# Performance work log

Hardware: AMD Instinct MI355X
Metric: run time of the kernel (lower is better)

The kernel has to match this reference:

```python
import jax, jax.numpy as jnp
import numpy as np

NUM_CODES = 512
DIM = 64
B, M = 32, 64


def setup_inputs() -> dict:
    key = jax.random.key(0)
    k1, k2 = jax.random.split(key)
    inputs = jax.random.normal(k1, (B, M, M, DIM), dtype=jnp.float32)
    # keras 'uniform' initializer is U(-0.05, 0.05)
    embeddings = jax.random.uniform(k2, (NUM_CODES, DIM), dtype=jnp.float32,
                                    minval=-0.05, maxval=0.05)
    return {"inputs": inputs, "embeddings": embeddings}


def reference(inputs, embeddings):
    l2_inputs = jnp.sum(inputs * inputs, axis=-1, keepdims=True)      # [B,M,M,1]
    l2_embeddings = jnp.sum(embeddings * embeddings, axis=-1)          # [K]
    dot = jnp.einsum('bhwd,kd->bhwk', inputs, embeddings)              # [B,M,M,K]
    distance = l2_inputs + l2_embeddings - 2.0 * dot                   # [B,M,M,K]
    codes = jnp.argmin(distance, axis=-1).astype(jnp.int32)            # [B,M,M]
    code_vecs = embeddings[codes]                                      # [B,M,M,D]
    return codes, code_vecs
```

## Files before the change

kernel.cpp:

```cpp
#include <hip/hip_runtime.h>

#define NUM_CODES 512
#define DIM 64
#define NPIX (32 * 64 * 64)
#define CT (NUM_CODES / 16)
#define BLK 256
#define NGRP 2
#define PPB 128

typedef __attribute__((ext_vector_type(8))) short bf16x8;
typedef __attribute__((ext_vector_type(4))) float f32x4;

__device__ __forceinline__ unsigned short f2bf(float f) {
    unsigned u = __float_as_uint(f);
    return (unsigned short)((u + 0x7fffu + ((u >> 16) & 1u)) >> 16);
}
__device__ __forceinline__ float bf2f(unsigned short h) {
    return __uint_as_float(((unsigned)h) << 16);
}

__global__ __launch_bounds__(256) void prep_kernel(
    const float* __restrict__ emb, unsigned short* __restrict__ AH,
    unsigned short* __restrict__ ALO, float* __restrict__ l2e,
    float* __restrict__ l2eh) {
    const int t = blockIdx.x * 256 + threadIdx.x;
    const int e0 = t * 4;
    const int c = e0 >> 6, d0 = e0 & 63;
    const float4 v = *(const float4*)(emb + c * DIM + d0);
    float f[4] = {-v.x, -v.y, -v.z, -v.w};
    unsigned short h[4], l[4];
#pragma unroll
    for (int i = 0; i < 4; ++i) {
        h[i] = f2bf(f[i]);
        l[i] = f2bf(f[i] - bf2f(h[i]));
    }
    const int ct = c >> 4, mr = c & 15, s = d0 >> 5, q = (d0 & 31) >> 3,
              j0 = d0 & 7;
    const int base = ((ct * 2 + s) * 64 + (q * 16 + mr)) * 8 + j0;
    *(ushort4*)(AH + base) = make_ushort4(h[0], h[1], h[2], h[3]);
    *(ushort4*)(ALO + base) = make_ushort4(l[0], l[1], l[2], l[3]);

    if (t < NUM_CODES) {
        const float* e = emb + t * DIM;
        float r[8];
#pragma unroll
        for (int j = 0; j < 8; ++j) {
            float w = e[j];
            r[j] = w * w;
        }
#pragma unroll
        for (int i = 8; i < DIM; i += 8)
#pragma unroll
            for (int j = 0; j < 8; ++j) {
                float w = e[i + j];
                r[j] += w * w;
            }
        float sv =
            ((r[0] + r[1]) + (r[2] + r[3])) + ((r[4] + r[5]) + (r[6] + r[7]));
        l2e[t] = sv;
        l2eh[t] = 0.5f * sv;
    }
}

__global__ __launch_bounds__(BLK, 4) void vq_main(
    const float* __restrict__ x_in, const unsigned short* __restrict__ AH,
    const unsigned short* __restrict__ ALO, const float* __restrict__ l2e,
    const float* __restrict__ l2eh, const float* __restrict__ emb,
    float* __restrict__ codes_out, float* __restrict__ vecs_out) {
    __shared__ float s_l2eh[NUM_CODES];
    __shared__ float s_l2ex[NUM_CODES];
    __shared__ int s_top[PPB][2];
    __shared__ int s_code[PPB];

    const int tid = threadIdx.x, lane = tid & 63, wave = tid >> 6;
    s_l2eh[tid] = l2eh[tid];
    s_l2eh[tid + 256] = l2eh[tid + 256];
    s_l2ex[tid] = l2e[tid];
    s_l2ex[tid + 256] = l2e[tid + 256];
    __syncthreads();

    const int p = lane & 15, q = lane >> 4;
    const int pw = blockIdx.x * PPB + wave * (16 * NGRP);

    bf16x8 bh0[NGRP], bl0[NGRP], bh1[NGRP], bl1[NGRP];
#pragma unroll
    for (int g = 0; g < NGRP; ++g) {
        const float* xb = x_in + (size_t)(pw + g * 16 + p) * DIM + q * 8;
        float4 u0 = *(const float4*)(xb);
        float4 u1 = *(const float4*)(xb + 4);
        float4 u2 = *(const float4*)(xb + 32);
        float4 u3 = *(const float4*)(xb + 36);
        float f0[8] = {u0.x, u0.y, u0.z, u0.w, u1.x, u1.y, u1.z, u1.w};
        float f1[8] = {u2.x, u2.y, u2.z, u2.w, u3.x, u3.y, u3.z, u3.w};
#pragma unroll
        for (int j = 0; j < 8; ++j) {
            unsigned short hh = f2bf(f0[j]);
            bh0[g][j] = (short)hh;
            bl0[g][j] = (short)f2bf(f0[j] - bf2f(hh));
            unsigned short h2 = f2bf(f1[j]);
            bh1[g][j] = (short)h2;
            bl1[g][j] = (short)f2bf(f1[j] - bf2f(h2));
        }
    }

    const int rowbase = q * 4;
    float d1[NGRP], d2[NGRP];
    int k1[NGRP], k2[NGRP];
#pragma unroll
    for (int g = 0; g < NGRP; ++g) {
        d1[g] = 3.4e38f;
        d2[g] = 3.4e38f;
        k1[g] = 0;
        k2[g] = 0;
    }

    const unsigned short* pAH = AH + lane * 8;
    const unsigned short* pAL = ALO + lane * 8;

    bf16x8 c0h = *(const bf16x8*)(pAH);
    bf16x8 c0l = *(const bf16x8*)(pAL);
    bf16x8 c1h = *(const bf16x8*)(pAH + 512);
    bf16x8 c1l = *(const bf16x8*)(pAL + 512);
    bf16x8 p0h = *(const bf16x8*)(pAH + 1024);
    bf16x8 p0l = *(const bf16x8*)(pAL + 1024);
    bf16x8 p1h = *(const bf16x8*)(pAH + 1024 + 512);
    bf16x8 p1l = *(const bf16x8*)(pAL + 1024 + 512);

#pragma unroll 4
    for (int ct = 0; ct < CT; ++ct) {
        const int nt = (ct + 2) & (CT - 1);
        const bf16x8 q0h = *(const bf16x8*)(pAH + nt * 1024);
        const bf16x8 q0l = *(const bf16x8*)(pAL + nt * 1024);
        const bf16x8 q1h = *(const bf16x8*)(pAH + nt * 1024 + 512);
        const bf16x8 q1l = *(const bf16x8*)(pAL + nt * 1024 + 512);

        const int kb = ct * 16 + rowbase;
        const f32x4 acc_init = *(const f32x4*)&s_l2eh[kb];

        f32x4 accA[NGRP], accB[NGRP];
        __builtin_amdgcn_s_setprio(1);
#pragma unroll
        for (int g = 0; g < NGRP; ++g) {
            f32x4 a = acc_init;
            a = __builtin_amdgcn_mfma_f32_16x16x32_bf16(c0h, bh0[g], a, 0, 0, 0);
            a = __builtin_amdgcn_mfma_f32_16x16x32_bf16(c0l, bh0[g], a, 0, 0, 0);
            a = __builtin_amdgcn_mfma_f32_16x16x32_bf16(c0h, bl0[g], a, 0, 0, 0);
            f32x4 b = {0.f, 0.f, 0.f, 0.f};
            b = __builtin_amdgcn_mfma_f32_16x16x32_bf16(c1h, bh1[g], b, 0, 0, 0);
            b = __builtin_amdgcn_mfma_f32_16x16x32_bf16(c1l, bh1[g], b, 0, 0, 0);
            b = __builtin_amdgcn_mfma_f32_16x16x32_bf16(c1h, bl1[g], b, 0, 0, 0);
            accA[g] = a;
            accB[g] = b;
        }
        __builtin_amdgcn_s_setprio(0);

#pragma unroll
        for (int g = 0; g < NGRP; ++g) {
#pragma unroll
            for (int r = 0; r < 4; ++r) {
                const float d = accA[g][r] + accB[g][r];
                const int kk = kb + r;
                const bool c = d < d1[g], c2 = d < d2[g];
                const float nd2 = __builtin_amdgcn_fmed3f(d1[g], d2[g], d);
                const int nk2 = c2 ? kk : k2[g];
                k2[g] = c ? k1[g] : nk2;
                k1[g] = c ? kk : k1[g];
                d2[g] = nd2;
                d1[g] = fminf(d1[g], d);
            }
        }

        c0h = p0h; c0l = p0l; c1h = p1h; c1l = p1l;
        p0h = q0h; p0l = q0l; p1h = q1h; p1l = q1l;
    }

#pragma unroll
    for (int g = 0; g < NGRP; ++g) {
        float a1 = d1[g], a2 = d2[g];
        int b1 = k1[g], b2 = k2[g];
#pragma unroll
        for (int off = 16; off <= 32; off <<= 1) {
            const float od1 = __shfl_xor(a1, off);
            const int ok1 = __shfl_xor(b1, off);
            const float od2 = __shfl_xor(a2, off);
            const int ok2 = __shfl_xor(b2, off);
            const bool c = od1 < a1;
            const float w1 = c ? od1 : a1;
            const int wk1 = c ? ok1 : b1;
            const float l1 = c ? a1 : od1;
            const int lk1 = c ? b1 : ok1;
            const bool cm = od2 < a2;
            const float m2 = cm ? od2 : a2;
            const int mk2 = cm ? ok2 : b2;
            const bool c3 = m2 < l1;
            a2 = c3 ? m2 : l1;
            b2 = c3 ? mk2 : lk1;
            a1 = w1;
            b1 = wk1;
        }
        if (lane < 16) {
            const int pb = wave * (16 * NGRP) + g * 16 + lane;
            s_top[pb][0] = b1;
            s_top[pb][1] = b2;
        }
    }
    __syncthreads();

    {
        const int pixloc = tid >> 1, which = tid & 1;
        const int pix = blockIdx.x * PPB + pixloc;
        const int k_me = s_top[pixloc][which];
        const float* xr = x_in + (size_t)pix * DIM;
        float x[DIM];
#pragma unroll
        for (int jj = 0; jj < 16; ++jj) {
            const float4 v = *(const float4*)(xr + jj * 4);
            x[4 * jj + 0] = v.x;
            x[4 * jj + 1] = v.y;
            x[4 * jj + 2] = v.z;
            x[4 * jj + 3] = v.w;
        }
        float r[8];
#pragma unroll
        for (int j = 0; j < 8; ++j) r[j] = x[j] * x[j];
#pragma unroll
        for (int i = 8; i < DIM; i += 8)
#pragma unroll
            for (int j = 0; j < 8; ++j) r[j] += x[i + j] * x[i + j];
        const float l2x =
            ((r[0] + r[1]) + (r[2] + r[3])) + ((r[4] + r[5]) + (r[6] + r[7]));

        const float* em = emb + (size_t)k_me * DIM;
        float acc = 0.f;
#pragma unroll
        for (int d = 0; d < DIM; ++d) acc = __builtin_fmaf(x[d], em[d], acc);
        const float d_me = (l2x + s_l2ex[k_me]) - 2.0f * acc;

        const float d_o = __shfl_xor(d_me, 1);
        const int k_o = __shfl_xor(k_me, 1);
        const int sel =
            (d_me < d_o || (d_me == d_o && k_me < k_o)) ? k_me : k_o;
        if (which == 0) {
            s_code[pixloc] = sel;
            codes_out[pix] = (float)sel;
        }
    }
    __syncthreads();

    const float4* emb4 = (const float4*)emb;
    float4* vout4 = (float4*)(vecs_out + (size_t)blockIdx.x * PPB * DIM);
#pragma unroll
    for (int it = 0; it < (PPB * DIM / 4) / BLK; ++it) {
        const int fidx = tid + it * BLK;
        const int pp = fidx >> 4, dd = fidx & 15;
        vout4[fidx] = emb4[(size_t)s_code[pp] * (DIM / 4) + dd];
    }
}

extern "C" void kernel_launch(void* const* d_in, const int* in_sizes, int n_in,
                              void* d_out, int out_size, void* d_ws,
                              size_t ws_size, hipStream_t stream) {
    const float* x_in = (const float*)d_in[0];
    const float* emb = (const float*)d_in[1];

    unsigned short* AH = (unsigned short*)d_ws;
    unsigned short* ALO = AH + NUM_CODES * DIM;
    float* l2e = (float*)(ALO + NUM_CODES * DIM);
    float* l2eh = l2e + NUM_CODES;

    float* codes_out = (float*)d_out;
    float* vecs_out = (float*)d_out + NPIX;

    hipLaunchKernelGGL(prep_kernel, dim3(32), dim3(256), 0, stream, emb, AH,
                       ALO, l2e, l2eh);
    hipLaunchKernelGGL(vq_main, dim3(NPIX / PPB), dim3(BLK), 0, stream, x_in,
                       AH, ALO, l2e, l2eh, emb, codes_out, vecs_out);
}
```

Measured before the change: 120.1 us.

## Switch to single-wave blocks with shuffle-based exchange, removing LDS and barriers

Each block becomes one 64-lane wave processing 16 pixels instead of four waves with two pixel groups each. Shared-memory staging of norms, top-2 candidates and codes is replaced by direct global loads of the code norms and cross-lane shuffles, which removes all block-level barriers. The intent is to cut synchronisation and LDS overhead and raise occupancy. In exchange, each codebook fragment loaded is reused across half as many pixels, so codebook reads double and each wave has less independent MFMA work to hide latency.

```diff
diff --git a/kernel.cpp b/kernel.cpp
--- a/kernel.cpp
+++ b/kernel.cpp
@@ -4,9 +4,8 @@
 #define DIM 64
 #define NPIX (32 * 64 * 64)
 #define CT (NUM_CODES / 16)
-#define BLK 256
-#define NGRP 2
-#define PPB 128
+#define BLK 64
+#define PPB 16
 
 typedef __attribute__((ext_vector_type(8))) short bf16x8;
 typedef __attribute__((ext_vector_type(4))) float f32x4;
@@ -62,30 +61,18 @@
     }
 }
 
-__global__ __launch_bounds__(BLK, 4) void vq_main(
+__global__ __launch_bounds__(BLK, 8) void vq_main(
     const float* __restrict__ x_in, const unsigned short* __restrict__ AH,
     const unsigned short* __restrict__ ALO, const float* __restrict__ l2e,
     const float* __restrict__ l2eh, const float* __restrict__ emb,
     float* __restrict__ codes_out, float* __restrict__ vecs_out) {
-    __shared__ float s_l2eh[NUM_CODES];
-    __shared__ float s_l2ex[NUM_CODES];
-    __shared__ int s_top[PPB][2];
-    __shared__ int s_code[PPB];
-
-    const int tid = threadIdx.x, lane = tid & 63, wave = tid >> 6;
-    s_l2eh[tid] = l2eh[tid];
-    s_l2eh[tid + 256] = l2eh[tid + 256];
-    s_l2ex[tid] = l2e[tid];
-    s_l2ex[tid + 256] = l2e[tid + 256];
-    __syncthreads();
-
+    const int lane = threadIdx.x;
     const int p = lane & 15, q = lane >> 4;
-    const int pw = blockIdx.x * PPB + wave * (16 * NGRP);
-
-    bf16x8 bh0[NGRP], bl0[NGRP], bh1[NGRP], bl1[NGRP];
-#pragma unroll
-    for (int g = 0; g < NGRP; ++g) {
-        const float* xb = x_in + (size_t)(pw + g * 16 + p) * DIM + q * 8;
+    const int pw = blockIdx.x * PPB;
+
+    bf16x8 bh0, bl0, bh1, bl1;
+    {
+        const float* xb = x_in + (size_t)(pw + p) * DIM + q * 8;
         float4 u0 = *(const float4*)(xb);
         float4 u1 = *(const float4*)(xb + 4);
         float4 u2 = *(const float4*)(xb + 32);
@@ -95,36 +82,32 @@
 #pragma unroll
         for (int j = 0; j < 8; ++j) {
             unsigned short hh = f2bf(f0[j]);
-            bh0[g][j] = (short)hh;
-            bl0[g][j] = (short)f2bf(f0[j] - bf2f(hh));
+            bh0[j] = (short)hh;
+            bl0[j] = (short)f2bf(f0[j] - bf2f(hh));
             unsigned short h2 = f2bf(f1[j]);
-            bh1[g][j] = (short)h2;
-            bl1[g][j] = (short)f2bf(f1[j] - bf2f(h2));
+            bh1[j] = (short)h2;
+            bl1[j] = (short)f2bf(f1[j] - bf2f(h2));
         }
     }
 
     const int rowbase = q * 4;
-    float d1[NGRP], d2[NGRP];
-    int k1[NGRP], k2[NGRP];
-#pragma unroll
-    for (int g = 0; g < NGRP; ++g) {
-        d1[g] = 3.4e38f;
-        d2[g] = 3.4e38f;
-        k1[g] = 0;
-        k2[g] = 0;
-    }
+    float d1 = 3.4e38f, d2 = 3.4e38f;
+    int k1 = 0, k2 = 0;
 
     const unsigned short* pAH = AH + lane * 8;
     const unsigned short* pAL = ALO + lane * 8;
+    const float* pL = l2eh + rowbase;
 
     bf16x8 c0h = *(const bf16x8*)(pAH);
     bf16x8 c0l = *(const bf16x8*)(pAL);
     bf16x8 c1h = *(const bf16x8*)(pAH + 512);
     bf16x8 c1l = *(const bf16x8*)(pAL + 512);
+    f32x4 ci = *(const f32x4*)(pL);
     bf16x8 p0h = *(const bf16x8*)(pAH + 1024);
     bf16x8 p0l = *(const bf16x8*)(pAL + 1024);
     bf16x8 p1h = *(const bf16x8*)(pAH + 1024 + 512);
     bf16x8 p1l = *(const bf16x8*)(pAL + 1024 + 512);
+    f32x4 pi = *(const f32x4*)(pL + 16);
 
 #pragma unroll 4
     for (int ct = 0; ct < CT; ++ct) {
@@ -133,51 +116,40 @@
         const bf16x8 q0l = *(const bf16x8*)(pAL + nt * 1024);
         const bf16x8 q1h = *(const bf16x8*)(pAH + nt * 1024 + 512);
         const bf16x8 q1l = *(const bf16x8*)(pAL + nt * 1024 + 512);
+        const f32x4 qi = *(const f32x4*)(pL + nt * 16);
+
+        __builtin_amdgcn_s_setprio(1);
+        f32x4 a = ci;
+        a = __builtin_amdgcn_mfma_f32_16x16x32_bf16(c0h, bh0, a, 0, 0, 0);
+        a = __builtin_amdgcn_mfma_f32_16x16x32_bf16(c0l, bh0, a, 0, 0, 0);
+        a = __builtin_amdgcn_mfma_f32_16x16x32_bf16(c0h, bl0, a, 0, 0, 0);
+        f32x4 b = {0.f, 0.f, 0.f, 0.f};
+        b = __builtin_amdgcn_mfma_f32_16x16x32_bf16(c1h, bh1, b, 0, 0, 0);
+        b = __builtin_amdgcn_mfma_f32_16x16x32_bf16(c1l, bh1, b, 0, 0, 0);
+        b = __builtin_amdgcn_mfma_f32_16x16x32_bf16(c1h, bl1, b, 0, 0, 0);
+        __builtin_amdgcn_s_setprio(0);
 
         const int kb = ct * 16 + rowbase;
-        const f32x4 acc_init = *(const f32x4*)&s_l2eh[kb];
-
-        f32x4 accA[NGRP], accB[NGRP];
-        __builtin_amdgcn_s_setprio(1);
-#pragma unroll
-        for (int g = 0; g < NGRP; ++g) {
-            f32x4 a = acc_init;
-            a = __builtin_amdgcn_mfma_f32_16x16x32_bf16(c0h, bh0[g], a, 0, 0, 0);
-            a = __builtin_amdgcn_mfma_f32_16x16x32_bf16(c0l, bh0[g], a, 0, 0, 0);
-            a = __builtin_amdgcn_mfma_f32_16x16x32_bf16(c0h, bl0[g], a, 0, 0, 0);
-            f32x4 b = {0.f, 0.f, 0.f, 0.f};
-            b = __builtin_amdgcn_mfma_f32_16x16x32_bf16(c1h, bh1[g], b, 0, 0, 0);
-            b = __builtin_amdgcn_mfma_f32_16x16x32_bf16(c1l, bh1[g], b, 0, 0, 0);
-            b = __builtin_amdgcn_mfma_f32_16x16x32_bf16(c1h, bl1[g], b, 0, 0, 0);
-            accA[g] = a;
-            accB[g] = b;
-        }
-        __builtin_amdgcn_s_setprio(0);
-
-#pragma unroll
-        for (int g = 0; g < NGRP; ++g) {
-#pragma unroll
-            for (int r = 0; r < 4; ++r) {
-                const float d = accA[g][r] + accB[g][r];
-                const int kk = kb + r;
-                const bool c = d < d1[g], c2 = d < d2[g];
-                const float nd2 = __builtin_amdgcn_fmed3f(d1[g], d2[g], d);
-                const int nk2 = c2 ? kk : k2[g];
-                k2[g] = c ? k1[g] : nk2;
-                k1[g] = c ? kk : k1[g];
-                d2[g] = nd2;
-                d1[g] = fminf(d1[g], d);
-            }
-        }
-
-        c0h = p0h; c0l = p0l; c1h = p1h; c1l = p1l;
-        p0h = q0h; p0l = q0l; p1h = q1h; p1l = q1l;
-    }
-
-#pragma unroll
-    for (int g = 0; g < NGRP; ++g) {
-        float a1 = d1[g], a2 = d2[g];
-        int b1 = k1[g], b2 = k2[g];
+#pragma unroll
+        for (int r = 0; r < 4; ++r) {
+            const float d = a[r] + b[r];
+            const int kk = kb + r;
+            const bool c = d < d1, c2 = d < d2;
+            const float nd2 = __builtin_amdgcn_fmed3f(d1, d2, d);
+            const int nk2 = c2 ? kk : k2;
+            k2 = c ? k1 : nk2;
+            k1 = c ? kk : k1;
+            d2 = nd2;
+            d1 = fminf(d1, d);
+        }
+
+        c0h = p0h; c0l = p0l; c1h = p1h; c1l = p1l; ci = pi;
+        p0h = q0h; p0l = q0l; p1h = q1h; p1l = q1l; pi = qi;
+    }
+
+    {
+        float a1 = d1, a2 = d2;
+        int b1 = k1, b2 = k2;
 #pragma unroll
         for (int off = 16; off <= 32; off <<= 1) {
             const float od1 = __shfl_xor(a1, off);
@@ -198,62 +170,69 @@
             a1 = w1;
             b1 = wk1;
         }
-        if (lane < 16) {
-            const int pb = wave * (16 * NGRP) + g * 16 + lane;
-            s_top[pb][0] = b1;
-            s_top[pb][1] = b2;
-        }
-    }
-    __syncthreads();
-
+        d1 = a1; k1 = b1;
+        d2 = a2; k2 = b2;
+    }
+
+    int sel;
     {
-        const int pixloc = tid >> 1, which = tid & 1;
-        const int pix = blockIdx.x * PPB + pixloc;
-        const int k_me = s_top[pixloc][which];
-        const float* xr = x_in + (size_t)pix * DIM;
-        float x[DIM];
-#pragma unroll
-        for (int jj = 0; jj < 16; ++jj) {
-            const float4 v = *(const float4*)(xr + jj * 4);
-            x[4 * jj + 0] = v.x;
-            x[4 * jj + 1] = v.y;
-            x[4 * jj + 2] = v.z;
-            x[4 * jj + 3] = v.w;
-        }
-        float r[8];
-#pragma unroll
-        for (int j = 0; j < 8; ++j) r[j] = x[j] * x[j];
-#pragma unroll
-        for (int i = 8; i < DIM; i += 8)
-#pragma unroll
-            for (int j = 0; j < 8; ++j) r[j] += x[i + j] * x[i + j];
-        const float l2x =
-            ((r[0] + r[1]) + (r[2] + r[3])) + ((r[4] + r[5]) + (r[6] + r[7]));
-
-        const float* em = emb + (size_t)k_me * DIM;
-        float acc = 0.f;
-#pragma unroll
-        for (int d = 0; d < DIM; ++d) acc = __builtin_fmaf(x[d], em[d], acc);
-        const float d_me = (l2x + s_l2ex[k_me]) - 2.0f * acc;
-
+        const int pixloc = (lane >> 1) & 15, which = lane & 1;
+        const int ka = __shfl(k1, pixloc);
+        const int kb2 = __shfl(k2, pixloc);
+        const int k_me = which ? kb2 : ka;
+        float d_me = 3.4e38f;
+        if (lane < 32) {
+            const int pix = pw + pixloc;
+            const float* xr = x_in + (size_t)pix * DIM;
+            const float* er = emb + (size_t)k_me * DIM;
+            float r[8];
+            float acc = 0.f;
+#pragma unroll
+            for (int i = 0; i < DIM; i += 8) {
+                const float4 xa = *(const float4*)(xr + i);
+                const float4 xb2 = *(const float4*)(xr + i + 4);
+                const float4 ea = *(const float4*)(er + i);
+                const float4 eb = *(const float4*)(er + i + 4);
+                if (i == 0) {
+                    r[0] = xa.x * xa.x; r[1] = xa.y * xa.y;
+                    r[2] = xa.z * xa.z; r[3] = xa.w * xa.w;
+                    r[4] = xb2.x * xb2.x; r[5] = xb2.y * xb2.y;
+                    r[6] = xb2.z * xb2.z; r[7] = xb2.w * xb2.w;
+                } else {
+                    r[0] += xa.x * xa.x; r[1] += xa.y * xa.y;
+                    r[2] += xa.z * xa.z; r[3] += xa.w * xa.w;
+                    r[4] += xb2.x * xb2.x; r[5] += xb2.y * xb2.y;
+                    r[6] += xb2.z * xb2.z; r[7] += xb2.w * xb2.w;
+                }
+                acc = __builtin_fmaf(xa.x, ea.x, acc);
+                acc = __builtin_fmaf(xa.y, ea.y, acc);
+                acc = __builtin_fmaf(xa.z, ea.z, acc);
+                acc = __builtin_fmaf(xa.w, ea.w, acc);
+                acc = __builtin_fmaf(xb2.x, eb.x, acc);
+                acc = __builtin_fmaf(xb2.y, eb.y, acc);
+                acc = __builtin_fmaf(xb2.z, eb.z, acc);
+                acc = __builtin_fmaf(xb2.w, eb.w, acc);
+            }
+            const float l2x = ((r[0] + r[1]) + (r[2] + r[3])) +
+                              ((r[4] + r[5]) + (r[6] + r[7]));
+            d_me = (l2x + l2e[k_me]) - 2.0f * acc;
+        }
         const float d_o = __shfl_xor(d_me, 1);
         const int k_o = __shfl_xor(k_me, 1);
-        const int sel =
-            (d_me < d_o || (d_me == d_o && k_me < k_o)) ? k_me : k_o;
-        if (which == 0) {
-            s_code[pixloc] = sel;
-            codes_out[pix] = (float)sel;
-        }
-    }
-    __syncthreads();
+        sel = (d_me < d_o || (d_me == d_o && k_me < k_o)) ? k_me : k_o;
+        if (lane < 32 && which == 0) {
+            codes_out[pw + pixloc] = (float)sel;
+        }
+    }
 
     const float4* emb4 = (const float4*)emb;
     float4* vout4 = (float4*)(vecs_out + (size_t)blockIdx.x * PPB * DIM);
 #pragma unroll
     for (int it = 0; it < (PPB * DIM / 4) / BLK; ++it) {
-        const int fidx = tid + it * BLK;
+        const int fidx = lane + it * BLK;
         const int pp = fidx >> 4, dd = fidx & 15;
-        vout4[fidx] = emb4[(size_t)s_code[pp] * (DIM / 4) + dd];
+        const int cpp = __shfl(sel, pp * 2);
+        vout4[fidx] = emb4[(size_t)cpp * (DIM / 4) + dd];
     }
 }
 
```

New measurement: 380.5 us. 3.17x slower.

## Stage codebook tiles through LDS with double-buffered global_load_lds

Applied to the files above, without the earlier changes.

Replaces per-wave register prefetching of codebook hi/lo bf16 fragments from global memory with a block-cooperative double-buffered LDS staging scheme using global_load_lds. Each wave loads one quarter of the next tile directly into shared memory, then all waves read fragments from LDS. The aim is to cut redundant global/L2 traffic, since every wave previously fetched the full codebook, and to free VGPRs. The cost is a vmcnt wait plus a block barrier on every code-tile iteration, which may stall the MFMA pipeline, and the unroll drops from 4 to 2.

```diff
diff --git a/kernel.cpp b/kernel.cpp
--- a/kernel.cpp
+++ b/kernel.cpp
@@ -71,12 +71,20 @@
     __shared__ float s_l2ex[NUM_CODES];
     __shared__ int s_top[PPB][2];
     __shared__ int s_code[PPB];
+    __shared__ short lbuf[2][2048];
 
     const int tid = threadIdx.x, lane = tid & 63, wave = tid >> 6;
     s_l2eh[tid] = l2eh[tid];
     s_l2eh[tid + 256] = l2eh[tid + 256];
     s_l2ex[tid] = l2e[tid];
     s_l2ex[tid + 256] = l2e[tid + 256];
+
+    const char* gsrc_base = (const char*)(wave < 2 ? AH : ALO) +
+                            (wave & 1) * 1024 + (size_t)lane * 16;
+
+    __builtin_amdgcn_global_load_lds(
+        (const unsigned int*)(gsrc_base),
+        (unsigned int*)&lbuf[0][wave * 512], 16, 0, 0);
     __syncthreads();
 
     const int p = lane & 15, q = lane >> 4;
@@ -114,25 +122,19 @@
         k2[g] = 0;
     }
 
-    const unsigned short* pAH = AH + lane * 8;
-    const unsigned short* pAL = ALO + lane * 8;
-
-    bf16x8 c0h = *(const bf16x8*)(pAH);
-    bf16x8 c0l = *(const bf16x8*)(pAL);
-    bf16x8 c1h = *(const bf16x8*)(pAH + 512);
-    bf16x8 c1l = *(const bf16x8*)(pAL + 512);
-    bf16x8 p0h = *(const bf16x8*)(pAH + 1024);
-    bf16x8 p0l = *(const bf16x8*)(pAL + 1024);
-    bf16x8 p1h = *(const bf16x8*)(pAH + 1024 + 512);
-    bf16x8 p1l = *(const bf16x8*)(pAL + 1024 + 512);
-
-#pragma unroll 4
+#pragma unroll 2
     for (int ct = 0; ct < CT; ++ct) {
-        const int nt = (ct + 2) & (CT - 1);
-        const bf16x8 q0h = *(const bf16x8*)(pAH + nt * 1024);
-        const bf16x8 q0l = *(const bf16x8*)(pAL + nt * 1024);
-        const bf16x8 q1h = *(const bf16x8*)(pAH + nt * 1024 + 512);
-        const bf16x8 q1l = *(const bf16x8*)(pAL + nt * 1024 + 512);
+        const int par = ct & 1;
+        const int nt = (ct + 1) & (CT - 1);
+
+        __builtin_amdgcn_global_load_lds(
+            (const unsigned int*)(gsrc_base + (size_t)nt * 2048),
+            (unsigned int*)&lbuf[par ^ 1][wave * 512], 16, 0, 0);
+
+        const bf16x8 a0h = *(const bf16x8*)&lbuf[par][lane * 8];
+        const bf16x8 a1h = *(const bf16x8*)&lbuf[par][512 + lane * 8];
+        const bf16x8 a0l = *(const bf16x8*)&lbuf[par][1024 + lane * 8];
+        const bf16x8 a1l = *(const bf16x8*)&lbuf[par][1536 + lane * 8];
 
         const int kb = ct * 16 + rowbase;
         const f32x4 acc_init = *(const f32x4*)&s_l2eh[kb];
@@ -142,13 +144,13 @@
 #pragma unroll
         for (int g = 0; g < NGRP; ++g) {
             f32x4 a = acc_init;
-            a = __builtin_amdgcn_mfma_f32_16x16x32_bf16(c0h, bh0[g], a, 0, 0, 0);
-            a = __builtin_amdgcn_mfma_f32_16x16x32_bf16(c0l, bh0[g], a, 0, 0, 0);
-            a = __builtin_amdgcn_mfma_f32_16x16x32_bf16(c0h, bl0[g], a, 0, 0, 0);
+            a = __builtin_amdgcn_mfma_f32_16x16x32_bf16(a0h, bh0[g], a, 0, 0, 0);
+            a = __builtin_amdgcn_mfma_f32_16x16x32_bf16(a0l, bh0[g], a, 0, 0, 0);
+            a = __builtin_amdgcn_mfma_f32_16x16x32_bf16(a0h, bl0[g], a, 0, 0, 0);
             f32x4 b = {0.f, 0.f, 0.f, 0.f};
-            b = __builtin_amdgcn_mfma_f32_16x16x32_bf16(c1h, bh1[g], b, 0, 0, 0);
-            b = __builtin_amdgcn_mfma_f32_16x16x32_bf16(c1l, bh1[g], b, 0, 0, 0);
-            b = __builtin_amdgcn_mfma_f32_16x16x32_bf16(c1h, bl1[g], b, 0, 0, 0);
+            b = __builtin_amdgcn_mfma_f32_16x16x32_bf16(a1h, bh1[g], b, 0, 0, 0);
+            b = __builtin_amdgcn_mfma_f32_16x16x32_bf16(a1l, bh1[g], b, 0, 0, 0);
+            b = __builtin_amdgcn_mfma_f32_16x16x32_bf16(a1h, bl1[g], b, 0, 0, 0);
             accA[g] = a;
             accB[g] = b;
         }
@@ -170,8 +172,9 @@
             }
         }
 
-        c0h = p0h; c0l = p0l; c1h = p1h; c1l = p1l;
-        p0h = q0h; p0l = q0l; p1h = q1h; p1l = q1l;
+        asm volatile("s_waitcnt vmcnt(0)" ::: "memory");
+        __builtin_amdgcn_s_barrier();
+        __builtin_amdgcn_sched_barrier(0);
     }
 
 #pragma unroll
```

Measured after the change: 120.9 us. No clear change (+0.7%).

## Software-pipeline MFMA distance tiles with previous tile's argmin update

Applied to the files above, without the earlier changes.

Restructures the code-tile loop so the MFMA results for tile ct are issued while the top-2 argmin comparison runs on tile ct-1's results. A prologue computes the first tile and an epilogue reduces the last one. The aim is to hide MFMA latency behind the VALU compare/select chain instead of stalling on each tile's accumulators. In exchange it holds extra accumulator registers, which may raise VGPR pressure and lower occupancy.

```diff
diff --git a/kernel.cpp b/kernel.cpp
--- a/kernel.cpp
+++ b/kernel.cpp
@@ -126,18 +126,15 @@
     bf16x8 p1h = *(const bf16x8*)(pAH + 1024 + 512);
     bf16x8 p1l = *(const bf16x8*)(pAL + 1024 + 512);
 
-#pragma unroll 4
-    for (int ct = 0; ct < CT; ++ct) {
-        const int nt = (ct + 2) & (CT - 1);
-        const bf16x8 q0h = *(const bf16x8*)(pAH + nt * 1024);
-        const bf16x8 q0l = *(const bf16x8*)(pAL + nt * 1024);
-        const bf16x8 q1h = *(const bf16x8*)(pAH + nt * 1024 + 512);
-        const bf16x8 q1l = *(const bf16x8*)(pAL + nt * 1024 + 512);
-
-        const int kb = ct * 16 + rowbase;
-        const f32x4 acc_init = *(const f32x4*)&s_l2eh[kb];
-
-        f32x4 accA[NGRP], accB[NGRP];
+    f32x4 pvA[NGRP], pvB[NGRP];
+
+    {
+        const bf16x8 q0h = *(const bf16x8*)(pAH + 2048);
+        const bf16x8 q0l = *(const bf16x8*)(pAL + 2048);
+        const bf16x8 q1h = *(const bf16x8*)(pAH + 2048 + 512);
+        const bf16x8 q1l = *(const bf16x8*)(pAL + 2048 + 512);
+
+        const f32x4 acc_init = *(const f32x4*)&s_l2eh[rowbase];
         __builtin_amdgcn_s_setprio(1);
 #pragma unroll
         for (int g = 0; g < NGRP; ++g) {
@@ -149,16 +146,48 @@
             b = __builtin_amdgcn_mfma_f32_16x16x32_bf16(c1h, bh1[g], b, 0, 0, 0);
             b = __builtin_amdgcn_mfma_f32_16x16x32_bf16(c1l, bh1[g], b, 0, 0, 0);
             b = __builtin_amdgcn_mfma_f32_16x16x32_bf16(c1h, bl1[g], b, 0, 0, 0);
-            accA[g] = a;
-            accB[g] = b;
+            pvA[g] = a;
+            pvB[g] = b;
         }
         __builtin_amdgcn_s_setprio(0);
 
+        c0h = p0h; c0l = p0l; c1h = p1h; c1l = p1l;
+        p0h = q0h; p0l = q0l; p1h = q1h; p1l = q1l;
+    }
+
+#pragma unroll 4
+    for (int ct = 1; ct < CT; ++ct) {
+        const int nt = (ct + 2) & (CT - 1);
+        const bf16x8 q0h = *(const bf16x8*)(pAH + nt * 1024);
+        const bf16x8 q0l = *(const bf16x8*)(pAL + nt * 1024);
+        const bf16x8 q1h = *(const bf16x8*)(pAH + nt * 1024 + 512);
+        const bf16x8 q1l = *(const bf16x8*)(pAL + nt * 1024 + 512);
+
+        const f32x4 acc_init = *(const f32x4*)&s_l2eh[ct * 16 + rowbase];
+
+        f32x4 cuA[NGRP], cuB[NGRP];
+        __builtin_amdgcn_s_setprio(1);
+#pragma unroll
+        for (int g = 0; g < NGRP; ++g) {
+            f32x4 a = acc_init;
+            a = __builtin_amdgcn_mfma_f32_16x16x32_bf16(c0h, bh0[g], a, 0, 0, 0);
+            a = __builtin_amdgcn_mfma_f32_16x16x32_bf16(c0l, bh0[g], a, 0, 0, 0);
+            a = __builtin_amdgcn_mfma_f32_16x16x32_bf16(c0h, bl0[g], a, 0, 0, 0);
+            f32x4 b = {0.f, 0.f, 0.f, 0.f};
+            b = __builtin_amdgcn_mfma_f32_16x16x32_bf16(c1h, bh1[g], b, 0, 0, 0);
+            b = __builtin_amdgcn_mfma_f32_16x16x32_bf16(c1l, bh1[g], b, 0, 0, 0);
+            b = __builtin_amdgcn_mfma_f32_16x16x32_bf16(c1h, bl1[g], b, 0, 0, 0);
+            cuA[g] = a;
+            cuB[g] = b;
+        }
+        __builtin_amdgcn_s_setprio(0);
+
+        const int kb = (ct - 1) * 16 + rowbase;
 #pragma unroll
         for (int g = 0; g < NGRP; ++g) {
 #pragma unroll
             for (int r = 0; r < 4; ++r) {
-                const float d = accA[g][r] + accB[g][r];
+                const float d = pvA[g][r] + pvB[g][r];
                 const int kk = kb + r;
                 const bool c = d < d1[g], c2 = d < d2[g];
                 const float nd2 = __builtin_amdgcn_fmed3f(d1[g], d2[g], d);
@@ -170,8 +199,32 @@
             }
         }
 
+#pragma unroll
+        for (int g = 0; g < NGRP; ++g) {
+            pvA[g] = cuA[g];
+            pvB[g] = cuB[g];
+        }
         c0h = p0h; c0l = p0l; c1h = p1h; c1l = p1l;
         p0h = q0h; p0l = q0l; p1h = q1h; p1l = q1l;
+    }
+
+    {
+        const int kb = (CT - 1) * 16 + rowbase;
+#pragma unroll
+        for (int g = 0; g < NGRP; ++g) {
+#pragma unroll
+            for (int r = 0; r < 4; ++r) {
+                const float d = pvA[g][r] + pvB[g][r];
+                const int kk = kb + r;
+                const bool c = d < d1[g], c2 = d < d2[g];
+                const float nd2 = __builtin_amdgcn_fmed3f(d1[g], d2[g], d);
+                const int nk2 = c2 ? kk : k2[g];
+                k2[g] = c ? k1[g] : nk2;
+                k1[g] = c ? kk : k1[g];
+                d2[g] = nd2;
+                d1[g] = fminf(d1[g], d);
+            }
+        }
     }
 
 #pragma unroll
```

Result: slower. 327.0 us (+172.4%).
